# Optimization experiments

Measured on AMD Instinct MI355X. Metric: run time of the kernel, lower is better.

Reference implementation:

```python
import jax, jax.numpy as jnp
import numpy as np
from jax import lax

DIM = 96
STYLE = 128
LAT = 8
K = 7
PAD = 3
B = 2
SP = 48
EPS = 1e-06


def setup_inputs() -> dict:
    key = jax.random.key(0)
    ks = jax.random.split(key, 20)
    d = {}
    d['x'] = jax.random.normal(ks[0], (B, DIM, SP, SP, SP), jnp.float32)
    d['s'] = jax.random.normal(ks[1], (B, STYLE), jnp.float32)
    # LayerNorm (channels_first) params
    d['ln_w'] = jnp.ones((DIM,), jnp.float32)
    d['ln_b'] = jnp.zeros((DIM,), jnp.float32)
    # layer scale
    d['gamma'] = jnp.full((1, DIM, 1, 1, 1), 1e-06, jnp.float32)
    sc = 0.02
    # depthwise hyperConv: groups=DIM -> in/groups = 1
    d['dw_fc_w'] = jax.random.normal(ks[2], (LAT, STYLE), jnp.float32) * sc
    d['dw_fc_b'] = jnp.zeros((LAT,), jnp.float32)
    d['dw_bank'] = jax.random.normal(ks[3], (DIM, 1 * K * K * K, LAT), jnp.float32) * sc
    d['dw_bias_bank'] = jax.random.normal(ks[4], (DIM, LAT), jnp.float32) * sc
    # pwconv1: dim -> 4*dim, 1x1x1
    d['pw1_fc_w'] = jax.random.normal(ks[5], (LAT, STYLE), jnp.float32) * sc
    d['pw1_fc_b'] = jnp.zeros((LAT,), jnp.float32)
    d['pw1_bank'] = jax.random.normal(ks[6], (4 * DIM, DIM, LAT), jnp.float32) * sc
    d['pw1_bias_bank'] = jax.random.normal(ks[7], (4 * DIM, LAT), jnp.float32) * sc
    # pwconv2: 4*dim -> dim, 1x1x1
    d['pw2_fc_w'] = jax.random.normal(ks[8], (LAT, STYLE), jnp.float32) * sc
    d['pw2_fc_b'] = jnp.zeros((LAT,), jnp.float32)
    d['pw2_bank'] = jax.random.normal(ks[9], (DIM, 4 * DIM, LAT), jnp.float32) * sc
    d['pw2_bias_bank'] = jax.random.normal(ks[10], (DIM, LAT), jnp.float32) * sc
    return d


def _dw_conv_one(xb, wb):
    # xb: (C, D, H, W) padded; wb: (C, 1, K, K, K); depthwise 'VALID' conv
    return lax.conv_general_dilated(
        xb[None], wb, window_strides=(1, 1, 1), padding='VALID',
        dimension_numbers=('NCDHW', 'OIDHW', 'NCDHW'),
        feature_group_count=DIM)[0]


def reference(x, s, ln_w, ln_b, gamma,
              dw_fc_w, dw_fc_b, dw_bank, dw_bias_bank,
              pw1_fc_w, pw1_fc_b, pw1_bank, pw1_bias_bank,
              pw2_fc_w, pw2_fc_b, pw2_bank, pw2_bias_bank):
    inp = x
    # zero-pad spatial dims by PAD
    xp = jnp.pad(x, ((0, 0), (0, 0), (PAD, PAD), (PAD, PAD), (PAD, PAD)))

    # --- depthwise hyperConv ---
    z = s @ dw_fc_w.T + dw_fc_b                         # (B, LAT)
    w_dw = jnp.einsum('okl,bl->bok', dw_bank, z)        # (B, C, K^3)
    w_dw = w_dw.reshape(x.shape[0], DIM, 1, K, K, K)
    b_dw = jnp.einsum('ol,bl->bo', dw_bias_bank, z)     # (B, C)
    h = jax.vmap(_dw_conv_one)(xp, w_dw) + b_dw[:, :, None, None, None]

    # --- LayerNorm channels_first over channel axis ---
    u = h.mean(axis=1, keepdims=True)
    v = ((h - u) ** 2).mean(axis=1, keepdims=True)
    h = (h - u) / jnp.sqrt(v + EPS)
    h = ln_w[None, :, None, None, None] * h + ln_b[None, :, None, None, None]

    # --- pointwise hyperConv 1 (1x1x1) as batched channel matmul ---
    z1 = s @ pw1_fc_w.T + pw1_fc_b
    w1 = jnp.einsum('ocl,bl->boc', pw1_bank, z1)        # (B, 4C, C)
    b1 = jnp.einsum('ol,bl->bo', pw1_bias_bank, z1)
    h = jnp.einsum('bcdhw,boc->bodhw', h, w1) + b1[:, :, None, None, None]

    # GELU (exact erf form, torch nn.GELU default)
    h = jax.nn.gelu(h, approximate=False)

    # --- pointwise hyperConv 2 ---
    z2 = s @ pw2_fc_w.T + pw2_fc_b
    w2 = jnp.einsum('ocl,bl->boc', pw2_bank, z2)        # (B, C, 4C)
    b2 = jnp.einsum('ol,bl->bo', pw2_bias_bank, z2)
    h = jnp.einsum('bcdhw,boc->bodhw', h, w2) + b2[:, :, None, None, None]

    return inp + gamma * h
```

## Files before the change

kernel.cpp:

```cpp
#include <hip/hip_runtime.h>
#include <math.h>

#define DIM   96
#define C4    384
#define STYLE 128
#define LAT   8
#define KK    7
#define BB    2
#define SPD   48
#define SP3   (SPD*SPD*SPD)
#define EPSV  1e-6f

#define XTS_E 30
#define YB    2
#define YSPAN 16
#define ZSPAN 8
#define XSPAN 24
#define YROWS 22
#define YROWP 23
#define ZPL   14

#define WS_Z    0
#define WS_WDW  64
#define WS_BDW  (WS_WDW + BB*DIM*343)
#define WS_W1   (WS_BDW + BB*DIM)
#define WS_B1   (WS_W1 + BB*C4*DIM)
#define WS_W2T  (WS_B1 + BB*C4)
#define WS_B2   (WS_W2T + BB*C4*DIM)
#define WS_H    (WS_B2 + BB*DIM)

typedef __attribute__((ext_vector_type(8))) __bf16 bf16x8;
typedef __attribute__((ext_vector_type(4))) __bf16 bf16x4;
typedef __attribute__((ext_vector_type(4))) float  f32x4;

__global__ __launch_bounds__(64) void kz(const float* __restrict__ s,
                                         const float* __restrict__ dwfw, const float* __restrict__ dwfb,
                                         const float* __restrict__ p1fw, const float* __restrict__ p1fb,
                                         const float* __restrict__ p2fw, const float* __restrict__ p2fb,
                                         float* __restrict__ ws) {
    int t = threadIdx.x;
    if (t >= 48) return;
    int which = t >> 4;
    int b = (t >> 3) & 1;
    int l = t & 7;
    const float* fw = (which == 0) ? dwfw : (which == 1) ? p1fw : p2fw;
    const float* fb = (which == 0) ? dwfb : (which == 1) ? p1fb : p2fb;
    float acc = fb[l];
    for (int k = 0; k < STYLE; ++k) acc += s[b*STYLE + k] * fw[l*STYLE + k];
    ws[WS_Z + which*16 + b*8 + l] = acc;
}

__global__ __launch_bounds__(256) void kw(const float* __restrict__ dwb,  const float* __restrict__ dwbb,
                                          const float* __restrict__ p1b,  const float* __restrict__ p1bb,
                                          const float* __restrict__ p2b,  const float* __restrict__ p2bb,
                                          float* __restrict__ ws) {
    const int n0 = BB*DIM*343;
    const int n1 = n0 + BB*DIM;
    const int n2 = n1 + BB*C4*DIM;
    const int n3 = n2 + BB*C4;
    const int n4 = n3 + BB*C4*DIM;
    const int n5 = n4 + BB*DIM;
    int i = blockIdx.x * blockDim.x + threadIdx.x;
    if (i >= n5) return;
    const float* zdw = ws + WS_Z;
    const float* z1  = ws + WS_Z + 16;
    const float* z2  = ws + WS_Z + 32;
    if (i < n0) {
        int b = i / (DIM*343); int r = i % (DIM*343); int c = r / 343; int k = r % 343;
        const float* bank = dwb + ((size_t)(c*343 + k))*LAT;
        const float* z = zdw + b*8;
        float a = 0.f;
        #pragma unroll
        for (int l = 0; l < LAT; ++l) a += bank[l]*z[l];
        ws[WS_WDW + i] = a;
    } else if (i < n1) {
        int j = i - n0; int b = j / DIM; int c = j % DIM;
        const float* z = zdw + b*8;
        float a = 0.f;
        #pragma unroll
        for (int l = 0; l < LAT; ++l) a += dwbb[c*LAT + l]*z[l];
        ws[WS_BDW + j] = a;
    } else if (i < n2) {
        int j = i - n1; int b = j / (C4*DIM); int r = j % (C4*DIM); int o = r / DIM; int c = r % DIM;
        const float* z = z1 + b*8;
        const float* bank = p1b + ((size_t)(o*DIM + c))*LAT;
        float a = 0.f;
        #pragma unroll
        for (int l = 0; l < LAT; ++l) a += bank[l]*z[l];
        ((__bf16*)(ws + WS_W1))[j] = (__bf16)a;
    } else if (i < n3) {
        int j = i - n2; int b = j / C4; int o = j % C4;
        const float* z = z1 + b*8;
        float a = 0.f;
        #pragma unroll
        for (int l = 0; l < LAT; ++l) a += p1bb[o*LAT + l]*z[l];
        ws[WS_B1 + j] = a;
    } else if (i < n4) {
        int j = i - n3; int b = j / (C4*DIM); int r = j % (C4*DIM); int o = r / C4; int c4 = r % C4;
        const float* z = z2 + b*8;
        const float* bank = p2b + ((size_t)(o*C4 + c4))*LAT;
        float a = 0.f;
        #pragma unroll
        for (int l = 0; l < LAT; ++l) a += bank[l]*z[l];
        ((__bf16*)(ws + WS_W2T))[j] = (__bf16)a;
    } else {
        int j = i - n4; int b = j / DIM; int o = j % DIM;
        const float* z = z2 + b*8;
        float a = 0.f;
        #pragma unroll
        for (int l = 0; l < LAT; ++l) a += p2bb[o*LAT + l]*z[l];
        ws[WS_B2 + j] = a;
    }
}

__global__ __launch_bounds__(192, 4) void kconv(const float* __restrict__ x, float* __restrict__ ws) {
    __shared__ __bf16 xt[ZPL*YROWP*XTS_E];
    int tid = threadIdx.x;
    int bx = blockIdx.x;
    int zt = bx / 6;
    int rt = bx % 6; int yt = rt >> 1; int xti = rt & 1;
    int c = blockIdx.y, b = blockIdx.z;
    int z0 = zt*ZSPAN, y0 = yt*YSPAN, x0 = xti*XSPAN;

    const float* xsrc = x + ((size_t)(b*DIM + c))*SP3;
    for (int i = tid; i < ZPL*YROWS*XTS_E; i += 192) {
        int iz = i / (YROWS*XTS_E); int r = i % (YROWS*XTS_E);
        int iy = r / XTS_E; int ix = r % XTS_E;
        int gz = z0 - 3 + iz, gy = y0 - 3 + iy, gx = x0 + ix - 3;
        float v = 0.f;
        if ((unsigned)gz < 48u && (unsigned)gy < 48u && (unsigned)gx < 48u)
            v = xsrc[(gz*SPD + gy)*SPD + gx];
        xt[(iz*YROWP + iy)*XTS_E + ix] = (__bf16)v;
    }
    __syncthreads();

    int tz = tid / 24; int rem = tid % 24; int ty = rem / 3; int tx = rem % 3;
    int xb = tx*8;
    float acc[YB][8];
    #pragma unroll
    for (int yl = 0; yl < YB; ++yl)
        #pragma unroll
        for (int j = 0; j < 8; ++j) acc[yl][j] = 0.f;

    const float* wsrc = ws + WS_WDW + ((size_t)(b*DIM + c))*343;

    #pragma unroll 1
    for (int dz = 0; dz < 7; ++dz) {
        float wv[7][7];
        const float* wp = wsrc + dz*49;
        #pragma unroll
        for (int dy = 0; dy < 7; ++dy)
            #pragma unroll
            for (int dx = 0; dx < 7; ++dx)
                wv[dy][dx] = wp[dy*7 + dx];

        const int zr = (tz + dz)*YROWP + ty*YB;
        #pragma unroll
        for (int r = 0; r < YB + 6; ++r) {
            const uint32_t* rowp = (const uint32_t*)&xt[(zr + r)*XTS_E + xb];
            uint32_t dw[7];
            #pragma unroll
            for (int k = 0; k < 7; ++k) dw[k] = rowp[k];
            float rr[14];
            #pragma unroll
            for (int k = 0; k < 7; ++k) {
                rr[2*k]   = __uint_as_float(dw[k] << 16);
                rr[2*k+1] = __uint_as_float(dw[k] & 0xffff0000u);
            }
            #pragma unroll
            for (int yl = 0; yl < YB; ++yl) {
                const int dy = r - yl;
                if (dy >= 0 && dy < 7) {
                    #pragma unroll
                    for (int dx = 0; dx < 7; ++dx)
                        #pragma unroll
                        for (int j = 0; j < 8; ++j)
                            acc[yl][j] += wv[dy][dx]*rr[dx+j];
                }
            }
        }
    }

    float bias = ws[WS_BDW + b*DIM + c];
    #pragma unroll
    for (int yl = 0; yl < YB; ++yl) {
        float* hdst = ws + WS_H + ((size_t)(b*DIM + c))*SP3
                    + (((z0+tz)*SPD + (y0 + ty*YB + yl))*SPD + (x0 + xb));
        #pragma unroll
        for (int j = 0; j < 8; ++j) hdst[j] = acc[yl][j] + bias;
    }
}

__global__ __launch_bounds__(256) void kpw(const float* __restrict__ x,
                                           const float* __restrict__ lnw, const float* __restrict__ lnb,
                                           const float* __restrict__ gamma,
                                           float* __restrict__ out, const float* __restrict__ ws) {
    __shared__ __align__(16) __bf16 Hn[64][104];
    __shared__ __align__(16) __bf16 G[64][392];
    __shared__ float2 redbuf[256];

    const int tid  = threadIdx.x;
    const int lane = tid & 63;
    const int w    = tid >> 6;
    const int b    = blockIdx.y;
    const int sp0  = blockIdx.x * 64;

    {
        const float* hp = ws + WS_H + (size_t)b*DIM*SP3 + (size_t)(w*24)*SP3 + sp0 + lane;
        float hv[24]; float s = 0.f, q = 0.f;
        #pragma unroll
        for (int i = 0; i < 24; ++i) {
            float v = hp[(size_t)i*SP3];
            hv[i] = v; s += v; q += v*v;
        }
        redbuf[w*64 + lane] = make_float2(s, q);
        __syncthreads();
        float2 r0 = redbuf[lane], r1 = redbuf[64+lane], r2 = redbuf[128+lane], r3 = redbuf[192+lane];
        float st = (r0.x+r1.x) + (r2.x+r3.x);
        float qt = (r0.y+r1.y) + (r2.y+r3.y);
        float mean = st * (1.f/96.f);
        float var  = qt * (1.f/96.f) - mean*mean;
        float rstd = rsqrtf(fmaxf(var, 0.f) + EPSV);
        #pragma unroll
        for (int i = 0; i < 24; ++i) {
            float nv = (hv[i] - mean)*rstd*lnw[w*24+i] + lnb[w*24+i];
            Hn[lane][w*24 + i] = (__bf16)nv;
        }
    }
    __syncthreads();

    const __bf16* W1b = (const __bf16*)(ws + WS_W1)  + (size_t)b*C4*DIM;
    const __bf16* W2b = (const __bf16*)(ws + WS_W2T) + (size_t)b*DIM*C4;
    const float*  b1  = ws + WS_B1 + b*C4;
    const float*  b2  = ws + WS_B2 + b*DIM;

    const int l16  = lane & 15;
    const int quad = lane >> 4;

    {
        const __bf16* bp = &Hn[w*16 + l16][quad*8];
        bf16x8 Bf0 = *(const bf16x8*)(bp);
        bf16x8 Bf1 = *(const bf16x8*)(bp + 32);
        bf16x8 Bf2 = *(const bf16x8*)(bp + 64);

        const __bf16* Arow = W1b + (size_t)l16*DIM + quad*8;
        #pragma unroll 1
        for (int mt = 0; mt < 24; ++mt) {
            const __bf16* ap = Arow + (size_t)mt*16*DIM;
            bf16x8 a0 = *(const bf16x8*)(ap);
            bf16x8 a1 = *(const bf16x8*)(ap + 32);
            bf16x8 a2 = *(const bf16x8*)(ap + 64);
            f32x4 acc = {0.f, 0.f, 0.f, 0.f};
            acc = __builtin_amdgcn_mfma_f32_16x16x32_bf16(a0, Bf0, acc, 0, 0, 0);
            acc = __builtin_amdgcn_mfma_f32_16x16x32_bf16(a1, Bf1, acc, 0, 0, 0);
            acc = __builtin_amdgcn_mfma_f32_16x16x32_bf16(a2, Bf2, acc, 0, 0, 0);
            int obase = mt*16 + quad*4;
            bf16x4 gv;
            #pragma unroll
            for (int r = 0; r < 4; ++r) {
                float t = acc[r] + b1[obase + r];
                float g = 0.5f*t*(1.f + erff(t*0.70710678f));
                gv[r] = (__bf16)g;
            }
            *(bf16x4*)&G[w*16 + l16][obase] = gv;
        }
    }
    __syncthreads();

    {
        bf16x8 Bg[12];
        const __bf16* gbp = &G[w*16 + l16][quad*8];
        #pragma unroll
        for (int ks = 0; ks < 12; ++ks)
            Bg[ks] = *(const bf16x8*)(gbp + ks*32);

        const __bf16* A2row = W2b + (size_t)l16*C4 + quad*8;
        const int j = w*16 + l16;
        const size_t base = (size_t)b*DIM*SP3 + sp0 + j;
        #pragma unroll 1
        for (int mt = 0; mt < 6; ++mt) {
            const __bf16* ap = A2row + (size_t)mt*16*C4;
            f32x4 acc = {0.f, 0.f, 0.f, 0.f};
            #pragma unroll
            for (int ks = 0; ks < 12; ++ks) {
                bf16x8 a = *(const bf16x8*)(ap + ks*32);
                acc = __builtin_amdgcn_mfma_f32_16x16x32_bf16(a, Bg[ks], acc, 0, 0, 0);
            }
            int obase = mt*16 + quad*4;
            #pragma unroll
            for (int r = 0; r < 4; ++r) {
                int o = obase + r;
                size_t idx = base + (size_t)o*SP3;
                float y = acc[r] + b2[o];
                out[idx] = x[idx] + gamma[o]*y;
            }
        }
    }
}

extern "C" void kernel_launch(void* const* d_in, const int* in_sizes, int n_in,
                              void* d_out, int out_size, void* d_ws, size_t ws_size,
                              hipStream_t stream) {
    const float* x      = (const float*)d_in[0];
    const float* s      = (const float*)d_in[1];
    const float* lnw    = (const float*)d_in[2];
    const float* lnb    = (const float*)d_in[3];
    const float* gamma  = (const float*)d_in[4];
    const float* dwfw   = (const float*)d_in[5];
    const float* dwfb   = (const float*)d_in[6];
    const float* dwbank = (const float*)d_in[7];
    const float* dwbb   = (const float*)d_in[8];
    const float* p1fw   = (const float*)d_in[9];
    const float* p1fb   = (const float*)d_in[10];
    const float* p1bank = (const float*)d_in[11];
    const float* p1bb   = (const float*)d_in[12];
    const float* p2fw   = (const float*)d_in[13];
    const float* p2fb   = (const float*)d_in[14];
    const float* p2bank = (const float*)d_in[15];
    const float* p2bb   = (const float*)d_in[16];
    float* ws  = (float*)d_ws;
    float* out = (float*)d_out;

    kz<<<1, 64, 0, stream>>>(s, dwfw, dwfb, p1fw, p1fb, p2fw, p2fb, ws);
    const int totW = BB*DIM*343 + BB*DIM + BB*C4*DIM + BB*C4 + BB*C4*DIM + BB*DIM;
    kw<<<(totW + 255)/256, 256, 0, stream>>>(dwbank, dwbb, p1bank, p1bb, p2bank, p2bb, ws);
    kconv<<<dim3(36, DIM, BB), 192, 0, stream>>>(x, ws);
    kpw<<<dim3(SP3/64, BB), 256, 0, stream>>>(x, lnw, lnb, gamma, out, ws);
}
```

Baseline: 681.9 us.

## Chunk hidden dimension in pointwise MLP to shrink LDS footprint

Splits the 384-wide hidden activation into four chunks of 96. Each chunk is computed, passed through GELU, staged in a small LDS buffer, and immediately accumulated into the second-matmul accumulators held in registers. The GELU staging buffer shrinks from 64x392 to 64x104 bf16, which should raise occupancy of the pointwise kernel. The cost is extra __syncthreads per chunk and 24 live accumulator floats per thread.

```diff
diff --git a/kernel.cpp b/kernel.cpp
--- a/kernel.cpp
+++ b/kernel.cpp
@@ -196,7 +196,7 @@
                                            const float* __restrict__ gamma,
                                            float* __restrict__ out, const float* __restrict__ ws) {
     __shared__ __align__(16) __bf16 Hn[64][104];
-    __shared__ __align__(16) __bf16 G[64][392];
+    __shared__ __align__(16) __bf16 Gq[64][104];
     __shared__ float2 redbuf[256];
 
     const int tid  = threadIdx.x;
@@ -237,16 +237,22 @@
     const int l16  = lane & 15;
     const int quad = lane >> 4;
 
-    {
-        const __bf16* bp = &Hn[w*16 + l16][quad*8];
-        bf16x8 Bf0 = *(const bf16x8*)(bp);
-        bf16x8 Bf1 = *(const bf16x8*)(bp + 32);
-        bf16x8 Bf2 = *(const bf16x8*)(bp + 64);
-
-        const __bf16* Arow = W1b + (size_t)l16*DIM + quad*8;
+    const __bf16* bp = &Hn[w*16 + l16][quad*8];
+    bf16x8 Bf0 = *(const bf16x8*)(bp);
+    bf16x8 Bf1 = *(const bf16x8*)(bp + 32);
+    bf16x8 Bf2 = *(const bf16x8*)(bp + 64);
+
+    float acc2[6][4];
+    #pragma unroll
+    for (int m = 0; m < 6; ++m)
+        #pragma unroll
+        for (int r = 0; r < 4; ++r) acc2[m][r] = 0.f;
+
+    #pragma unroll 1
+    for (int q = 0; q < 4; ++q) {
         #pragma unroll 1
-        for (int mt = 0; mt < 24; ++mt) {
-            const __bf16* ap = Arow + (size_t)mt*16*DIM;
+        for (int mtl = 0; mtl < 6; ++mtl) {
+            const __bf16* ap = W1b + (size_t)((q*6 + mtl)*16 + l16)*DIM + quad*8;
             bf16x8 a0 = *(const bf16x8*)(ap);
             bf16x8 a1 = *(const bf16x8*)(ap + 32);
             bf16x8 a2 = *(const bf16x8*)(ap + 64);
@@ -254,46 +260,47 @@
             acc = __builtin_amdgcn_mfma_f32_16x16x32_bf16(a0, Bf0, acc, 0, 0, 0);
             acc = __builtin_amdgcn_mfma_f32_16x16x32_bf16(a1, Bf1, acc, 0, 0, 0);
             acc = __builtin_amdgcn_mfma_f32_16x16x32_bf16(a2, Bf2, acc, 0, 0, 0);
-            int obase = mt*16 + quad*4;
+            int og = (q*6 + mtl)*16 + quad*4;
+            int ol = mtl*16 + quad*4;
             bf16x4 gv;
             #pragma unroll
             for (int r = 0; r < 4; ++r) {
-                float t = acc[r] + b1[obase + r];
+                float t = acc[r] + b1[og + r];
                 float g = 0.5f*t*(1.f + erff(t*0.70710678f));
                 gv[r] = (__bf16)g;
             }
-            *(bf16x4*)&G[w*16 + l16][obase] = gv;
-        }
-    }
-    __syncthreads();
-
-    {
-        bf16x8 Bg[12];
-        const __bf16* gbp = &G[w*16 + l16][quad*8];
-        #pragma unroll
-        for (int ks = 0; ks < 12; ++ks)
-            Bg[ks] = *(const bf16x8*)(gbp + ks*32);
-
-        const __bf16* A2row = W2b + (size_t)l16*C4 + quad*8;
-        const int j = w*16 + l16;
-        const size_t base = (size_t)b*DIM*SP3 + sp0 + j;
+            *(bf16x4*)&Gq[w*16 + l16][ol] = gv;
+        }
+        __syncthreads();
+
         #pragma unroll 1
-        for (int mt = 0; mt < 6; ++mt) {
-            const __bf16* ap = A2row + (size_t)mt*16*C4;
-            f32x4 acc = {0.f, 0.f, 0.f, 0.f};
-            #pragma unroll
-            for (int ks = 0; ks < 12; ++ks) {
-                bf16x8 a = *(const bf16x8*)(ap + ks*32);
-                acc = __builtin_amdgcn_mfma_f32_16x16x32_bf16(a, Bg[ks], acc, 0, 0, 0);
+        for (int ksl = 0; ksl < 3; ++ksl) {
+            bf16x8 Bg = *(const bf16x8*)&Gq[w*16 + l16][ksl*32 + quad*8];
+            const int kbase = q*96 + ksl*32 + quad*8;
+            #pragma unroll
+            for (int mt2 = 0; mt2 < 6; ++mt2) {
+                const __bf16* ap2 = W2b + (size_t)(mt2*16 + l16)*C4 + kbase;
+                bf16x8 a = *(const bf16x8*)(ap2);
+                f32x4 c = {acc2[mt2][0], acc2[mt2][1], acc2[mt2][2], acc2[mt2][3]};
+                c = __builtin_amdgcn_mfma_f32_16x16x32_bf16(a, Bg, c, 0, 0, 0);
+                acc2[mt2][0] = c[0]; acc2[mt2][1] = c[1];
+                acc2[mt2][2] = c[2]; acc2[mt2][3] = c[3];
             }
-            int obase = mt*16 + quad*4;
-            #pragma unroll
-            for (int r = 0; r < 4; ++r) {
-                int o = obase + r;
-                size_t idx = base + (size_t)o*SP3;
-                float y = acc[r] + b2[o];
-                out[idx] = x[idx] + gamma[o]*y;
-            }
+        }
+        __syncthreads();
+    }
+
+    const int j = w*16 + l16;
+    const size_t base = (size_t)b*DIM*SP3 + sp0 + j;
+    #pragma unroll
+    for (int mt2 = 0; mt2 < 6; ++mt2) {
+        int obase = mt2*16 + quad*4;
+        #pragma unroll
+        for (int r = 0; r < 4; ++r) {
+            int o = obase + r;
+            size_t idx = base + (size_t)o*SP3;
+            float y = acc2[mt2][r] + b2[o];
+            out[idx] = x[idx] + gamma[o]*y;
         }
     }
 }
```

Result: faster. 625.5 us (-8.3%).
